# Performance work log

Hardware: AMD Instinct MI355X
Metric: run time of the kernel (lower is better)

## Reference

```python
import jax, jax.numpy as jnp
import numpy as np

N = 50000
E_RAND = 800000
F_IN = 256
F_OUT = 256
ALPHA = 0.2  # LeakyReLU negative slope


def setup_inputs() -> dict:
    key = jax.random.key(0)
    k1, k2, k3, k4 = jax.random.split(key, 4)
    x = jax.random.normal(k1, (N, F_IN), dtype=jnp.float32)
    # random edges + self-loops so every row has at least one edge (avoids div by 0)
    edge_rand = jax.random.randint(k2, (2, E_RAND), 0, N)
    loops = jnp.arange(N)
    edge = jnp.concatenate([edge_rand, jnp.stack([loops, loops])], axis=1)  # [2, 850000]
    W = jax.random.normal(k3, (F_IN, F_OUT), dtype=jnp.float32) * 0.05
    a = jax.random.normal(k4, (2 * F_OUT,), dtype=jnp.float32) * 0.05
    return {"x": x, "edge": edge, "W": W, "a": a}


def reference(x, edge, W, a):
    # x: [N, F_in], edge: [2, E] (row = dst/aggregation index per torch.sparse.mm(a, h))
    n = x.shape[0]
    f_out = W.shape[1]
    h = x @ W  # [N, F_out]
    src, dst = edge[0], edge[1]
    # a @ [h_src; h_dst] decomposes into two per-node dot products (no [E, 2F] concat)
    s = h @ a[:f_out]   # [N]
    t = h @ a[f_out:]   # [N]
    logit = s[src] + t[dst]                                  # [E]
    e = jnp.exp(-jax.nn.leaky_relu(logit, ALPHA))            # [E]
    rowsum = jax.ops.segment_sum(e, src, num_segments=n)     # [N]
    msg = e[:, None] * h[dst]                                # [E, F_out]
    h_prime = jax.ops.segment_sum(msg, src, num_segments=n)  # [N, F_out]
    h_prime = h_prime / rowsum[:, None]
    return jax.nn.relu(h_prime)  # concat=True path
```

## Files before the change

### kernel.cpp

```cpp
#include <hip/hip_runtime.h>
#include <hip/hip_fp16.h>

#define FDIM 256
#define ALPHA 0.2f
#define PAD 48
#define CURSTRIDE 16

typedef _Float16 half8 __attribute__((ext_vector_type(8)));
typedef float floatx4 __attribute__((ext_vector_type(4)));
typedef int intx2 __attribute__((ext_vector_type(2)));

__global__ __launch_bounds__(256) void prep_w(const float* __restrict__ W,
                                              _Float16* __restrict__ wswz) {
  const int g = blockIdx.x * 256 + threadIdx.x;
  const int kc = g >> 11, L = g & 2047;
  const int n = L >> 3, c = L & 7;
  half8 hv;
#pragma unroll
  for (int j = 0; j < 8; ++j)
    hv[j] = (_Float16)W[(size_t)(kc * 64 + c * 8 + j) * 256 + n];
  *(half8*)(wswz + (size_t)g * 8) = hv;
}

#define HT_STRIDE 132
__global__ __launch_bounds__(256, 5) void gemm_mfma(
    const float* __restrict__ x, const _Float16* __restrict__ wswz,
    const float* __restrict__ a, _Float16* __restrict__ h,
    float* __restrict__ s, float* __restrict__ t, int M) {
  __shared__ __align__(16) _Float16 smem[64 * HT_STRIDE];
  _Float16* As = smem;
  const int tid = threadIdx.x;
  const int w = tid >> 6, l = tid & 63;
  const int l15 = l & 15, q = l >> 4;
  const int nh = blockIdx.x & 1;
  const int row0 = (blockIdx.x >> 1) * 64;

  floatx4 acc[4][2];
#pragma unroll
  for (int mt = 0; mt < 4; ++mt)
#pragma unroll
    for (int nt = 0; nt < 2; ++nt) acc[mt][nt] = (floatx4){0.f, 0.f, 0.f, 0.f};

  const int id0 = tid, id1 = 256 + tid;
  const int m0 = id0 >> 3, c0 = (id0 & 7) ^ (m0 & 7);
  const int m1 = id1 >> 3, c1 = (id1 & 7) ^ (m1 & 7);
  const int r0 = row0 + m0, r1 = row0 + m1;

  float4 pf[2][2];
  auto loadA = [&](int kc) {
    pf[0][0] = pf[0][1] = pf[1][0] = pf[1][1] = make_float4(0.f, 0.f, 0.f, 0.f);
    if (r0 < M) {
      const float4* p = (const float4*)(x + (size_t)r0 * 256 + kc * 64 + c0 * 8);
      pf[0][0] = p[0];
      pf[0][1] = p[1];
    }
    if (r1 < M) {
      const float4* p = (const float4*)(x + (size_t)r1 * 256 + kc * 64 + c1 * 8);
      pf[1][0] = p[0];
      pf[1][1] = p[1];
    }
  };
  auto storeA = [&]() {
#pragma unroll
    for (int hf = 0; hf < 2; ++hf) {
      half8 hv;
      hv[0] = (_Float16)pf[hf][0].x; hv[1] = (_Float16)pf[hf][0].y;
      hv[2] = (_Float16)pf[hf][0].z; hv[3] = (_Float16)pf[hf][0].w;
      hv[4] = (_Float16)pf[hf][1].x; hv[5] = (_Float16)pf[hf][1].y;
      hv[6] = (_Float16)pf[hf][1].z; hv[7] = (_Float16)pf[hf][1].w;
      *(half8*)(As + (size_t)(hf * 256 + tid) * 8) = hv;
    }
  };

  loadA(0);
  for (int kc = 0; kc < 4; ++kc) {
    storeA();
    half8 bf[2][2];
#pragma unroll
    for (int ks = 0; ks < 2; ++ks) {
      const int c = ks * 4 + q;
#pragma unroll
      for (int nt = 0; nt < 2; ++nt) {
        const int n = nh * 128 + w * 32 + nt * 16 + l15;
        bf[ks][nt] = *(const half8*)(wswz + (size_t)(kc * 2048 + n * 8 + c) * 8);
      }
    }
    __syncthreads();
    if (kc < 3) loadA(kc + 1);
#pragma unroll
    for (int ks = 0; ks < 2; ++ks) {
      const int c = ks * 4 + q;
      half8 af[4];
#pragma unroll
      for (int mt = 0; mt < 4; ++mt) {
        const int m = mt * 16 + l15;
        af[mt] = *(const half8*)(As + (size_t)(m * 8 + (c ^ (m & 7))) * 8);
      }
#pragma unroll
      for (int mt = 0; mt < 4; ++mt)
#pragma unroll
        for (int nt = 0; nt < 2; ++nt)
          acc[mt][nt] = __builtin_amdgcn_mfma_f32_16x16x32_f16(
              af[mt], bf[ks][nt], acc[mt][nt], 0, 0, 0);
    }
    __syncthreads();
  }

#pragma unroll
  for (int mt = 0; mt < 4; ++mt)
#pragma unroll
    for (int nt = 0; nt < 2; ++nt)
#pragma unroll
      for (int r = 0; r < 4; ++r)
        smem[(size_t)(mt * 16 + q * 4 + r) * HT_STRIDE + w * 32 + nt * 16 +
             l15] = (_Float16)acc[mt][nt][r];
  __syncthreads();

  const int w16 = tid >> 4;
  const int colh = (tid & 15) * 8;
#pragma unroll
  for (int p = 0; p < 4; ++p) {
    const int rl = p * 16 + w16;
    const int row = row0 + rl;
    if (row < M)
      *(half8*)(h + (size_t)row * 256 + nh * 128 + colh) =
          *(const half8*)(smem + (size_t)rl * HT_STRIDE + colh);
  }

  const int r8 = tid >> 2, seg = tid & 3;
  float sp = 0.f, tp = 0.f;
#pragma unroll
  for (int c8 = 0; c8 < 4; ++c8) {
    const int col = seg * 32 + c8 * 8;
    const int acol = nh * 128 + col;
    const half8 hv = *(const half8*)(smem + (size_t)r8 * HT_STRIDE + col);
    const float4 a0 = *(const float4*)(a + acol);
    const float4 a1 = *(const float4*)(a + acol + 4);
    const float4 b0 = *(const float4*)(a + 256 + acol);
    const float4 b1 = *(const float4*)(a + 256 + acol + 4);
    sp += (float)hv[0] * a0.x + (float)hv[1] * a0.y + (float)hv[2] * a0.z +
          (float)hv[3] * a0.w + (float)hv[4] * a1.x + (float)hv[5] * a1.y +
          (float)hv[6] * a1.z + (float)hv[7] * a1.w;
    tp += (float)hv[0] * b0.x + (float)hv[1] * b0.y + (float)hv[2] * b0.z +
          (float)hv[3] * b0.w + (float)hv[4] * b1.x + (float)hv[5] * b1.y +
          (float)hv[6] * b1.z + (float)hv[7] * b1.w;
  }
  sp += __shfl_xor(sp, 1);
  sp += __shfl_xor(sp, 2);
  tp += __shfl_xor(tp, 1);
  tp += __shfl_xor(tp, 2);
  if (seg == 0 && row0 + r8 < M) {
    atomicAdd(&s[row0 + r8], sp);
    atomicAdd(&t[row0 + r8], tp);
  }
}

__global__ __launch_bounds__(256) void scatter_kernel(
    const int* __restrict__ edge, int* __restrict__ rsc,
    const float* __restrict__ s, const float* __restrict__ t,
    int2* __restrict__ sde, int E) {
  const int e = blockIdx.x * 256 + threadIdx.x;
  if (e < E) {
    const int src = edge[e];
    const int dst = edge[E + e];
    const float logit = s[src] + t[dst];
    const float lr = logit > 0.f ? logit : ALPHA * logit;
    const float ev = __expf(-lr);
    const int off = atomicAdd(&rsc[src * CURSTRIDE], 1);
    if (off < PAD)
      sde[(size_t)src * PAD + off] = make_int2(dst, __float_as_int(ev));
  }
}

__global__ __launch_bounds__(256) void agg_kernel(
    const _Float16* __restrict__ h, const int* __restrict__ rsc,
    const int2* __restrict__ sde, float* __restrict__ out, int n) {
  const int w = threadIdx.x >> 6, l = threadIdx.x & 63;
  const int row = blockIdx.x * 4 + w;
  if (row >= n) return;
  int cnt = rsc[row * CURSTRIDE];
  cnt = cnt < PAD ? cnt : PAD;
  const int start = row * PAD;
  const int end = start + cnt;
  const int half = l >> 5;
  const int lh = l & 31;
  const size_t fo = (size_t)lh * 8;
  float acc[8] = {};
  float rs = 0.f;
  int j = start;
  for (; j + 8 <= end; j += 8) {
#pragma unroll
    for (int u = 0; u < 4; ++u) {
      const int2 p = sde[j + u * 2 + half];
      const half8 v = *(const half8*)(h + (size_t)p.x * 256 + fo);
      const float e = __int_as_float(p.y);
      rs += e;
#pragma unroll
      for (int k = 0; k < 8; ++k) acc[k] += e * (float)v[k];
    }
  }
  for (; j < end; j += 2) {
    const int idx = j + half;
    const bool valid = idx < end;
    const int2 p = valid ? sde[idx] : make_int2(0, 0);
    const half8 v = *(const half8*)(h + (size_t)p.x * 256 + fo);
    const float e = valid ? __int_as_float(p.y) : 0.f;
    rs += e;
#pragma unroll
    for (int k = 0; k < 8; ++k) acc[k] += e * (float)v[k];
  }
  rs += __shfl_xor(rs, 32);
#pragma unroll
  for (int k = 0; k < 8; ++k) acc[k] += __shfl_xor(acc[k], 32);
  const float inv = 1.f / rs;
  float4 o;
#pragma unroll
  for (int k = 0; k < 4; ++k) {
    const float vv = acc[half * 4 + k] * inv;
    (&o.x)[k] = vv > 0.f ? vv : 0.f;
  }
  *(float4*)(out + (size_t)row * 256 + lh * 8 + half * 4) = o;
}

extern "C" void kernel_launch(void* const* d_in, const int* in_sizes, int n_in,
                              void* d_out, int out_size, void* d_ws,
                              size_t ws_size, hipStream_t stream) {
  const float* x = (const float*)d_in[0];
  const int* edge = (const int*)d_in[1];
  const float* W = (const float*)d_in[2];
  const float* a = (const float*)d_in[3];
  float* out = (float*)d_out;
  const int N = in_sizes[0] / FDIM;
  const int E = in_sizes[1] / 2;
  const int NBLK_GEMM = ((N + 63) / 64) * 2;

  _Float16* h = (_Float16*)d_ws;
  _Float16* wswz = h + (size_t)N * FDIM;
  float* s = (float*)(wswz + 8192 * 8);
  float* t = s + N;
  int* rsc = (int*)(t + N);
  int2* sde = (int2*)(rsc + (size_t)N * CURSTRIDE);

  hipMemsetAsync(s, 0, ((size_t)N * (2 + CURSTRIDE)) * sizeof(int), stream);

  prep_w<<<32, 256, 0, stream>>>(W, wswz);
  gemm_mfma<<<NBLK_GEMM, 256, 0, stream>>>(x, wswz, a, h, s, t, N);
  scatter_kernel<<<(E + 255) / 256, 256, 0, stream>>>(edge, rsc, s, t, sde, E);
  agg_kernel<<<(N + 3) / 4, 256, 0, stream>>>(h, rsc, sde, out, N);
}
```

Measured before the change: 242.6 us.

## Precompute W·a to get s,t from x and fuse scatter into GEMM launch

Attention scores s and t are now computed as x·(W a_src) and x·(W a_dst), using vectors precomputed in a merged prep kernel that also zeroes the row counters in place of the memset. A small st_kernel computes s,t straight from x, so the scatter no longer depends on the GEMM and the two run as disjoint block ranges of one launch. This removes the atomics and epilogue from the GEMM, drops a launch and a memset, and lets scatter overlap GEMM work. In exchange x is read twice, s and t are computed in fp32 from x rather than from fp16 h, and the GEMM occupancy hint is raised.

After: 323.2 us. 1.33x slower.

```diff
diff --git a/kernel.cpp b/kernel.cpp
--- a/kernel.cpp
+++ b/kernel.cpp
@@ -10,23 +10,92 @@
 typedef float floatx4 __attribute__((ext_vector_type(4)));
 typedef int intx2 __attribute__((ext_vector_type(2)));
 
-__global__ __launch_bounds__(256) void prep_w(const float* __restrict__ W,
-                                              _Float16* __restrict__ wswz) {
-  const int g = blockIdx.x * 256 + threadIdx.x;
-  const int kc = g >> 11, L = g & 2047;
-  const int n = L >> 3, c = L & 7;
-  half8 hv;
-#pragma unroll
-  for (int j = 0; j < 8; ++j)
-    hv[j] = (_Float16)W[(size_t)(kc * 64 + c * 8 + j) * 256 + n];
-  *(half8*)(wswz + (size_t)g * 8) = hv;
+__global__ __launch_bounds__(256) void prep_all(
+    const float* __restrict__ W, _Float16* __restrict__ wswz,
+    const float* __restrict__ a, float* __restrict__ wa,
+    float* __restrict__ wb, int* __restrict__ rsc, int n16) {
+  const int b = blockIdx.x;
+  if (b < 32) {
+    const int g = b * 256 + threadIdx.x;
+    const int kc = g >> 11, L = g & 2047;
+    const int n = L >> 3, c = L & 7;
+    half8 hv;
+#pragma unroll
+    for (int j = 0; j < 8; ++j)
+      hv[j] = (_Float16)W[(size_t)(kc * 64 + c * 8 + j) * 256 + n];
+    *(half8*)(wswz + (size_t)g * 8) = hv;
+  } else if (b == 32) {
+    const int k = threadIdx.x;
+    const float4* wr = (const float4*)(W + (size_t)k * 256);
+    const float4* ar = (const float4*)a;
+    const float4* br = (const float4*)(a + 256);
+    float va = 0.f, vb = 0.f;
+#pragma unroll
+    for (int i = 0; i < 64; ++i) {
+      const float4 wv = wr[i];
+      const float4 av = ar[i];
+      const float4 bv = br[i];
+      va += wv.x * av.x + wv.y * av.y + wv.z * av.z + wv.w * av.w;
+      vb += wv.x * bv.x + wv.y * bv.y + wv.z * bv.z + wv.w * bv.w;
+    }
+    wa[k] = va;
+    wb[k] = vb;
+  } else {
+    const int i = (b - 33) * 1024 + threadIdx.x * 4;
+    if (i < n16) *(int4*)(rsc + i) = make_int4(0, 0, 0, 0);
+  }
+}
+
+__global__ __launch_bounds__(256) void st_kernel(
+    const float* __restrict__ x, const float* __restrict__ wa,
+    const float* __restrict__ wb, float* __restrict__ s,
+    float* __restrict__ t, int M) {
+  const int tid = threadIdx.x;
+  const int row = blockIdx.x * 64 + (tid >> 2);
+  const int seg = tid & 3;
+  if (row >= M) return;
+  const float4* xp = (const float4*)(x + (size_t)row * 256 + seg * 64);
+  const float4* ap = (const float4*)(wa + seg * 64);
+  const float4* bp = (const float4*)(wb + seg * 64);
+  float sp = 0.f, tp = 0.f;
+#pragma unroll
+  for (int i = 0; i < 16; ++i) {
+    const float4 xv = xp[i];
+    const float4 av = ap[i];
+    const float4 bv = bp[i];
+    sp += xv.x * av.x + xv.y * av.y + xv.z * av.z + xv.w * av.w;
+    tp += xv.x * bv.x + xv.y * bv.y + xv.z * bv.z + xv.w * bv.w;
+  }
+  sp += __shfl_xor(sp, 1);
+  sp += __shfl_xor(sp, 2);
+  tp += __shfl_xor(tp, 1);
+  tp += __shfl_xor(tp, 2);
+  if (seg == 0) {
+    s[row] = sp;
+    t[row] = tp;
+  }
 }
 
 #define HT_STRIDE 132
-__global__ __launch_bounds__(256, 5) void gemm_mfma(
+__global__ __launch_bounds__(256, 8) void gemm_scatter(
     const float* __restrict__ x, const _Float16* __restrict__ wswz,
-    const float* __restrict__ a, _Float16* __restrict__ h,
-    float* __restrict__ s, float* __restrict__ t, int M) {
+    _Float16* __restrict__ h, int M, const int* __restrict__ edge,
+    int* __restrict__ rsc, const float* __restrict__ s,
+    const float* __restrict__ t, int2* __restrict__ sde, int E, int nblk) {
+  if ((int)blockIdx.x >= nblk) {
+    const int e = ((int)blockIdx.x - nblk) * 256 + threadIdx.x;
+    if (e < E) {
+      const int src = edge[e];
+      const int dst = edge[E + e];
+      const float logit = s[src] + t[dst];
+      const float lr = logit > 0.f ? logit : ALPHA * logit;
+      const float ev = __expf(-lr);
+      const int off = atomicAdd(&rsc[src * CURSTRIDE], 1);
+      if (off < PAD)
+        sde[(size_t)src * PAD + off] = make_int2(dst, __float_as_int(ev));
+    }
+    return;
+  }
   __shared__ __align__(16) _Float16 smem[64 * HT_STRIDE];
   _Float16* As = smem;
   const int tid = threadIdx.x;
@@ -125,50 +194,6 @@
     if (row < M)
       *(half8*)(h + (size_t)row * 256 + nh * 128 + colh) =
           *(const half8*)(smem + (size_t)rl * HT_STRIDE + colh);
-  }
-
-  const int r8 = tid >> 2, seg = tid & 3;
-  float sp = 0.f, tp = 0.f;
-#pragma unroll
-  for (int c8 = 0; c8 < 4; ++c8) {
-    const int col = seg * 32 + c8 * 8;
-    const int acol = nh * 128 + col;
-    const half8 hv = *(const half8*)(smem + (size_t)r8 * HT_STRIDE + col);
-    const float4 a0 = *(const float4*)(a + acol);
-    const float4 a1 = *(const float4*)(a + acol + 4);
-    const float4 b0 = *(const float4*)(a + 256 + acol);
-    const float4 b1 = *(const float4*)(a + 256 + acol + 4);
-    sp += (float)hv[0] * a0.x + (float)hv[1] * a0.y + (float)hv[2] * a0.z +
-          (float)hv[3] * a0.w + (float)hv[4] * a1.x + (float)hv[5] * a1.y +
-          (float)hv[6] * a1.z + (float)hv[7] * a1.w;
-    tp += (float)hv[0] * b0.x + (float)hv[1] * b0.y + (float)hv[2] * b0.z +
-          (float)hv[3] * b0.w + (float)hv[4] * b1.x + (float)hv[5] * b1.y +
-          (float)hv[6] * b1.z + (float)hv[7] * b1.w;
-  }
-  sp += __shfl_xor(sp, 1);
-  sp += __shfl_xor(sp, 2);
-  tp += __shfl_xor(tp, 1);
-  tp += __shfl_xor(tp, 2);
-  if (seg == 0 && row0 + r8 < M) {
-    atomicAdd(&s[row0 + r8], sp);
-    atomicAdd(&t[row0 + r8], tp);
-  }
-}
-
-__global__ __launch_bounds__(256) void scatter_kernel(
-    const int* __restrict__ edge, int* __restrict__ rsc,
-    const float* __restrict__ s, const float* __restrict__ t,
-    int2* __restrict__ sde, int E) {
-  const int e = blockIdx.x * 256 + threadIdx.x;
-  if (e < E) {
-    const int src = edge[e];
-    const int dst = edge[E + e];
-    const float logit = s[src] + t[dst];
-    const float lr = logit > 0.f ? logit : ALPHA * logit;
-    const float ev = __expf(-lr);
-    const int off = atomicAdd(&rsc[src * CURSTRIDE], 1);
-    if (off < PAD)
-      sde[(size_t)src * PAD + off] = make_int2(dst, __float_as_int(ev));
   }
 }
 
@@ -233,18 +258,22 @@
   const int N = in_sizes[0] / FDIM;
   const int E = in_sizes[1] / 2;
   const int NBLK_GEMM = ((N + 63) / 64) * 2;
+  const int NBLK_SCAT = (E + 255) / 256;
+  const int N16 = N * CURSTRIDE;
+  const int NBLK_ZERO = (N16 + 1023) / 1024;
 
   _Float16* h = (_Float16*)d_ws;
   _Float16* wswz = h + (size_t)N * FDIM;
-  float* s = (float*)(wswz + 8192 * 8);
+  float* wa = (float*)(wswz + 8192 * 8);
+  float* wb = wa + 256;
+  float* s = wb + 256;
   float* t = s + N;
   int* rsc = (int*)(t + N);
   int2* sde = (int2*)(rsc + (size_t)N * CURSTRIDE);
 
-  hipMemsetAsync(s, 0, ((size_t)N * (2 + CURSTRIDE)) * sizeof(int), stream);
-
-  prep_w<<<32, 256, 0, stream>>>(W, wswz);
-  gemm_mfma<<<NBLK_GEMM, 256, 0, stream>>>(x, wswz, a, h, s, t, N);
-  scatter_kernel<<<(E + 255) / 256, 256, 0, stream>>>(edge, rsc, s, t, sde, E);
+  prep_all<<<33 + NBLK_ZERO, 256, 0, stream>>>(W, wswz, a, wa, wb, rsc, N16);
+  st_kernel<<<(N + 63) / 64, 256, 0, stream>>>(x, wa, wb, s, t, N);
+  gemm_scatter<<<NBLK_GEMM + NBLK_SCAT, 256, 0, stream>>>(
+      x, wswz, h, N, edge, rsc, s, t, sde, E, NBLK_GEMM);
   agg_kernel<<<(N + 3) / 4, 256, 0, stream>>>(h, rsc, sde, out, N);
 }
```

## Fuse GAT pipeline into one cooperative persistent kernel with grid syncs

Applied to the files above, without the earlier changes.

Replaces the memset plus four separate kernel launches with a single cooperative persistent kernel. It runs W prep and zeroing, the GEMM, the edge scatter and the aggregation as grid-stride phases separated by grid.sync. The aim is to remove launch gaps and tail effects between stages. In exchange, every stage is capped at the occupancy-limited grid (at most 2048 blocks), grid-wide barriers have a cost, and the scatter and aggregation phases inherit the GEMM's launch bounds. A fallback path launches the stages as separate kernels.

Measured after the change: 591.5 us. 2.44x slower.

```diff
diff --git a/kernel.cpp b/kernel.cpp
--- a/kernel.cpp
+++ b/kernel.cpp
@@ -1,18 +1,21 @@
 #include <hip/hip_runtime.h>
 #include <hip/hip_fp16.h>
+#include <hip/hip_cooperative_groups.h>
+
+namespace cg = cooperative_groups;
 
 #define FDIM 256
 #define ALPHA 0.2f
 #define PAD 48
 #define CURSTRIDE 16
+#define HT_STRIDE 132
 
 typedef _Float16 half8 __attribute__((ext_vector_type(8)));
 typedef float floatx4 __attribute__((ext_vector_type(4)));
-typedef int intx2 __attribute__((ext_vector_type(2)));
-
-__global__ __launch_bounds__(256) void prep_w(const float* __restrict__ W,
-                                              _Float16* __restrict__ wswz) {
-  const int g = blockIdx.x * 256 + threadIdx.x;
+
+__device__ __forceinline__ void wswz_item(int b, const float* __restrict__ W,
+                                          _Float16* __restrict__ wswz) {
+  const int g = b * 256 + threadIdx.x;
   const int kc = g >> 11, L = g & 2047;
   const int n = L >> 3, c = L & 7;
   half8 hv;
@@ -22,18 +25,25 @@
   *(half8*)(wswz + (size_t)g * 8) = hv;
 }
 
-#define HT_STRIDE 132
-__global__ __launch_bounds__(256, 5) void gemm_mfma(
-    const float* __restrict__ x, const _Float16* __restrict__ wswz,
-    const float* __restrict__ a, _Float16* __restrict__ h,
-    float* __restrict__ s, float* __restrict__ t, int M) {
+__device__ __forceinline__ void zero_item(int b, int* __restrict__ z,
+                                          int nwords) {
+  const int i = b * 1024 + threadIdx.x * 4;
+  if (i < nwords) *(int4*)(z + i) = make_int4(0, 0, 0, 0);
+}
+
+__device__ __forceinline__ void gemm_tile(int tile, const float* __restrict__ x,
+                                          const _Float16* __restrict__ wswz,
+                                          const float* __restrict__ a,
+                                          _Float16* __restrict__ h,
+                                          float* __restrict__ s,
+                                          float* __restrict__ t, int M) {
   __shared__ __align__(16) _Float16 smem[64 * HT_STRIDE];
   _Float16* As = smem;
   const int tid = threadIdx.x;
   const int w = tid >> 6, l = tid & 63;
   const int l15 = l & 15, q = l >> 4;
-  const int nh = blockIdx.x & 1;
-  const int row0 = (blockIdx.x >> 1) * 64;
+  const int nh = tile & 1;
+  const int row0 = (tile >> 1) * 64;
 
   floatx4 acc[4][2];
 #pragma unroll
@@ -127,13 +137,13 @@
           *(const half8*)(smem + (size_t)rl * HT_STRIDE + colh);
   }
 
-  const int r8 = tid >> 2, seg = tid & 3;
+  const int r8_ = tid >> 2, seg = tid & 3;
   float sp = 0.f, tp = 0.f;
 #pragma unroll
   for (int c8 = 0; c8 < 4; ++c8) {
     const int col = seg * 32 + c8 * 8;
     const int acol = nh * 128 + col;
-    const half8 hv = *(const half8*)(smem + (size_t)r8 * HT_STRIDE + col);
+    const half8 hv = *(const half8*)(smem + (size_t)r8_ * HT_STRIDE + col);
     const float4 a0 = *(const float4*)(a + acol);
     const float4 a1 = *(const float4*)(a + acol + 4);
     const float4 b0 = *(const float4*)(a + 256 + acol);
@@ -149,17 +159,19 @@
   sp += __shfl_xor(sp, 2);
   tp += __shfl_xor(tp, 1);
   tp += __shfl_xor(tp, 2);
-  if (seg == 0 && row0 + r8 < M) {
-    atomicAdd(&s[row0 + r8], sp);
-    atomicAdd(&t[row0 + r8], tp);
-  }
-}
-
-__global__ __launch_bounds__(256) void scatter_kernel(
-    const int* __restrict__ edge, int* __restrict__ rsc,
-    const float* __restrict__ s, const float* __restrict__ t,
-    int2* __restrict__ sde, int E) {
-  const int e = blockIdx.x * 256 + threadIdx.x;
+  if (seg == 0 && row0 + r8_ < M) {
+    atomicAdd(&s[row0 + r8_], sp);
+    atomicAdd(&t[row0 + r8_], tp);
+  }
+  __syncthreads();
+}
+
+__device__ __forceinline__ void scatter_chunk(int c, const int* __restrict__ edge,
+                                              int* __restrict__ rsc,
+                                              const float* __restrict__ s,
+                                              const float* __restrict__ t,
+                                              int2* __restrict__ sde, int E) {
+  const int e = c * 256 + threadIdx.x;
   if (e < E) {
     const int src = edge[e];
     const int dst = edge[E + e];
@@ -172,11 +184,12 @@
   }
 }
 
-__global__ __launch_bounds__(256) void agg_kernel(
-    const _Float16* __restrict__ h, const int* __restrict__ rsc,
-    const int2* __restrict__ sde, float* __restrict__ out, int n) {
+__device__ __forceinline__ void agg_group(int g, const _Float16* __restrict__ h,
+                                          const int* __restrict__ rsc,
+                                          const int2* __restrict__ sde,
+                                          float* __restrict__ out, int n) {
   const int w = threadIdx.x >> 6, l = threadIdx.x & 63;
-  const int row = blockIdx.x * 4 + w;
+  const int row = g * 4 + w;
   if (row >= n) return;
   int cnt = rsc[row * CURSTRIDE];
   cnt = cnt < PAD ? cnt : PAD;
@@ -222,6 +235,60 @@
   *(float4*)(out + (size_t)row * 256 + lh * 8 + half * 4) = o;
 }
 
+__global__ __launch_bounds__(256, 5) void gat_mega(
+    const float* __restrict__ x, const int* __restrict__ edge,
+    const float* __restrict__ W, const float* __restrict__ a,
+    _Float16* __restrict__ wswz, _Float16* __restrict__ h,
+    float* __restrict__ s, float* __restrict__ t, int* __restrict__ rsc,
+    int2* __restrict__ sde, float* __restrict__ out, int N_, int E_, int nZ,
+    int nGemm, int nScat, int nAgg) {
+  cg::grid_group grid = cg::this_grid();
+  const int nb = gridDim.x;
+  const int nA = 32 + nZ;
+  for (int it = blockIdx.x; it < nA; it += nb) {
+    if (it < 32) wswz_item(it, W, wswz);
+    else zero_item(it - 32, (int*)s, 18 * N_);
+  }
+  __threadfence();
+  grid.sync();
+  for (int it = blockIdx.x; it < nGemm; it += nb)
+    gemm_tile(it, x, wswz, a, h, s, t, N_);
+  __threadfence();
+  grid.sync();
+  for (int it = blockIdx.x; it < nScat; it += nb)
+    scatter_chunk(it, edge, rsc, s, t, sde, E_);
+  __threadfence();
+  grid.sync();
+  for (int it = blockIdx.x; it < nAgg; it += nb)
+    agg_group(it, h, rsc, sde, out, N_);
+}
+
+__global__ __launch_bounds__(256) void k_prep(const float* __restrict__ W,
+                                              _Float16* __restrict__ wswz,
+                                              int* __restrict__ z, int nwords) {
+  if (blockIdx.x < 32) wswz_item(blockIdx.x, W, wswz);
+  else zero_item(blockIdx.x - 32, z, nwords);
+}
+__global__ __launch_bounds__(256, 5) void k_gemm(
+    const float* __restrict__ x, const _Float16* __restrict__ wswz,
+    const float* __restrict__ a, _Float16* __restrict__ h,
+    float* __restrict__ s, float* __restrict__ t, int M) {
+  gemm_tile(blockIdx.x, x, wswz, a, h, s, t, M);
+}
+__global__ __launch_bounds__(256) void k_scat(const int* __restrict__ edge,
+                                              int* __restrict__ rsc,
+                                              const float* __restrict__ s,
+                                              const float* __restrict__ t,
+                                              int2* __restrict__ sde, int E) {
+  scatter_chunk(blockIdx.x, edge, rsc, s, t, sde, E);
+}
+__global__ __launch_bounds__(256) void k_agg(const _Float16* __restrict__ h,
+                                             const int* __restrict__ rsc,
+                                             const int2* __restrict__ sde,
+                                             float* __restrict__ out, int n) {
+  agg_group(blockIdx.x, h, rsc, sde, out, n);
+}
+
 extern "C" void kernel_launch(void* const* d_in, const int* in_sizes, int n_in,
                               void* d_out, int out_size, void* d_ws,
                               size_t ws_size, hipStream_t stream) {
@@ -230,9 +297,12 @@
   const float* W = (const float*)d_in[2];
   const float* a = (const float*)d_in[3];
   float* out = (float*)d_out;
-  const int N = in_sizes[0] / FDIM;
-  const int E = in_sizes[1] / 2;
-  const int NBLK_GEMM = ((N + 63) / 64) * 2;
+  int N = in_sizes[0] / FDIM;
+  int E = in_sizes[1] / 2;
+  int NZ = (18 * N + 1023) / 1024;
+  int NGEMM = ((N + 63) / 64) * 2;
+  int NSCAT = (E + 255) / 256;
+  int NAGG = (N + 3) / 4;
 
   _Float16* h = (_Float16*)d_ws;
   _Float16* wswz = h + (size_t)N * FDIM;
@@ -241,10 +311,30 @@
   int* rsc = (int*)(t + N);
   int2* sde = (int2*)(rsc + (size_t)N * CURSTRIDE);
 
-  hipMemsetAsync(s, 0, ((size_t)N * (2 + CURSTRIDE)) * sizeof(int), stream);
-
-  prep_w<<<32, 256, 0, stream>>>(W, wswz);
-  gemm_mfma<<<NBLK_GEMM, 256, 0, stream>>>(x, wswz, a, h, s, t, N);
-  scatter_kernel<<<(E + 255) / 256, 256, 0, stream>>>(edge, rsc, s, t, sde, E);
-  agg_kernel<<<(N + 3) / 4, 256, 0, stream>>>(h, rsc, sde, out, N);
-}
+  static int coopGrid = -2;
+  if (coopGrid == -2) {
+    int maxb = 0;
+    hipError_t oe =
+        hipOccupancyMaxActiveBlocksPerMultiprocessor(&maxb, gat_mega, 256, 0);
+    coopGrid = (oe == hipSuccess && maxb > 0) ? maxb * 256 : -1;
+    if (coopGrid > 2048) coopGrid = 2048;
+  }
+  bool launched = false;
+  if (coopGrid > 0) {
+    void* args[] = {&x, &edge, &W, &a, &wswz, &h, &s, &t, &rsc, &sde,
+                    &out, &N, &E, &NZ, &NGEMM, &NSCAT, &NAGG};
+    hipError_t err = hipLaunchCooperativeKernel(
+        (const void*)gat_mega, dim3(coopGrid), dim3(256), args, 0, stream);
+    if (err == hipSuccess) {
+      launched = true;
+    } else {
+      coopGrid = -1;
+    }
+  }
+  if (!launched) {
+    k_prep<<<32 + NZ, 256, 0, stream>>>(W, wswz, (int*)s, 18 * N);
+    k_gemm<<<NGEMM, 256, 0, stream>>>(x, wswz, a, h, s, t, N);
+    k_scat<<<NSCAT, 256, 0, stream>>>(edge, rsc, s, t, sde, E);
+    k_agg<<<NAGG, 256, 0, stream>>>(h, rsc, sde, out, N);
+  }
+}
```
